# Performance work log

Hardware: AMD Instinct MI355X
Metric: run time of the kernel (lower is better)

## Reference

```python
import jax, jax.numpy as jnp
import numpy as np
from jax import lax

MARGIN_1 = 0.3
ALPHA_1 = 0.5
B, D = 256, 512
N_CLASSES = 32


def setup_inputs() -> dict:
    key = jax.random.key(0)
    k1, k2, k3 = jax.random.split(key, 3)
    feature = jax.random.normal(k1, (B, D), dtype=jnp.float32)
    sub = jax.random.randint(k2, (B,), 0, 2, dtype=jnp.int64)
    targets = jax.random.randint(k3, (B,), 0, N_CLASSES, dtype=jnp.int64)
    return {"feature": feature, "sub": sub, "targets": targets}


def _masked_softmax(logits, mask):
    # softmax over last axis restricted to `mask`; rows with empty mask -> all zeros
    # (matches torch behavior where an empty gather yields a zero transition matrix)
    neg = jnp.where(mask, logits, -jnp.inf)
    m = jnp.max(neg, axis=-1, keepdims=True)
    m = jnp.where(jnp.isfinite(m), m, 0.0)
    e = jnp.where(mask, jnp.exp(logits - m), 0.0)
    s = jnp.sum(e, axis=-1, keepdims=True)
    return e / jnp.maximum(s, 1e-30)


def _masked_mean(v, m):
    cnt = jnp.maximum(jnp.sum(m), 1).astype(v.dtype)
    return jnp.sum(jnp.where(m, v, 0.0)) / cnt


def _transition_loss(feature, sub, targets, margin_1, alpha_1):
    n = feature.shape[0]
    sim = feature @ feature.T  # [B,B], reused for every anchor

    def trans(mask_r, mask_c):
        # ab: rows -> mask_c columns; ba: rows -> mask_r columns.
        # Columns outside the mask are exactly 0, so the matmul only mixes
        # the same subset entries as torch's gathered mm, embedded in [B,B].
        ab = _masked_softmax(sim, mask_c[None, :])  # [B,B]
        ba = _masked_softmax(sim, mask_r[None, :])  # [B,B]
        tr = ab @ ba  # valid on rows/cols in mask_r
        return jnp.sqrt(jnp.clip(tr, 1e-12))

    def body(acc, i):
        is_pos = targets == targets[i]  # includes i itself
        is_neg = ~is_pos
        intra = sub == sub[i]
        cross = ~intra
        mpi = is_pos & intra
        mpc = is_pos & cross
        mni = is_neg & intra
        mnc = is_neg & cross
        trans_pos = trans(mpi, mpc)
        trans_neg = trans(mni, mnc)
        loss_ap = _masked_mean(jnp.clip(trans_neg + (margin_1 - alpha_1), 0.0),
                               mni[:, None] & mni[None, :])
        loss_an = _masked_mean(jnp.clip(alpha_1 - trans_pos, 0.0),
                               mpi[:, None] & mpi[None, :])
        return acc + loss_ap + loss_an, None

    total, _ = lax.scan(body, jnp.float32(0.0), jnp.arange(n))
    return total / n


def reference(feature, sub, targets):
    # NB: the torch module computes normalize(feature) into `x` but never uses it;
    # the loss consumes the raw `feature`, so we do the same.
    return _transition_loss(feature, sub, targets, MARGIN_1, ALPHA_1)
```

## Files before the change

### kernel.cpp

```cpp
#include <hip/hip_runtime.h>
#include <hip/hip_bf16.h>
#include <math.h>


constexpr int kB = 256;
constexpr int kD = 512;
constexpr float NEG_BIG = -3.4e38f;

typedef _Float16 f16x8 __attribute__((ext_vector_type(8)));
typedef float f32x16 __attribute__((ext_vector_type(16)));

constexpr int O_SIM = 0;
constexpr int O_M   = 262144;
constexpr int O_L   = 327680;
constexpr int O_IDX = 393216;
constexpr int O_CNT = 524288;
constexpr int O_MI  = 525312;
constexpr int O_MS  = 527360;

constexpr int XB_Q   = 43520;
constexpr int XB_E   = XB_Q + 1024;
constexpr int XB_F   = XB_E + 1024;
constexpr int XB_IK  = XB_F + 1024;
constexpr int XB_IR  = XB_IK + 512;
constexpr int XB_ROW = XB_IR + 512;
constexpr int XB_RED = XB_ROW + 8320;
constexpr int K2_LDS = XB_RED + 32;

__global__ __launch_bounds__(512)
void simStatsKernel(const float* __restrict__ f, const int* __restrict__ tgt,
                    const int* __restrict__ sub, float* __restrict__ sim,
                    float* __restrict__ Mv, float* __restrict__ Lv,
                    unsigned short* __restrict__ idxAll, int* __restrict__ cnt4,
                    int4* __restrict__ metaI, float* __restrict__ metaS,
                    float* __restrict__ out) {
  __shared__ float frow[2][512];
  __shared__ float panel[2][260];
  const int tid = threadIdx.x, lane = tid & 63, wave = tid >> 6;
  const int r0 = blockIdx.x * 2;
  if (tid < 256)
    ((float4*)frow)[tid] = ((const float4*)(f + (size_t)r0 * kD))[tid];
  __syncthreads();
  {
    const float4 a00 = *(const float4*)&frow[0][lane * 8];
    const float4 a01 = *(const float4*)&frow[0][lane * 8 + 4];
    const float4 a10 = *(const float4*)&frow[1][lane * 8];
    const float4 a11 = *(const float4*)&frow[1][lane * 8 + 4];
#pragma unroll 4
    for (int j = 0; j < 32; j++) {
      const int c = (wave << 5) | j;
      const float* fc = f + (size_t)c * kD + lane * 8;
      const float4 b0 = *(const float4*)fc;
      const float4 b1 = *(const float4*)(fc + 4);
      float d0 = 0.f, d1 = 0.f;
      d0 = fmaf(a00.x, b0.x, d0); d1 = fmaf(a10.x, b0.x, d1);
      d0 = fmaf(a00.y, b0.y, d0); d1 = fmaf(a10.y, b0.y, d1);
      d0 = fmaf(a00.z, b0.z, d0); d1 = fmaf(a10.z, b0.z, d1);
      d0 = fmaf(a00.w, b0.w, d0); d1 = fmaf(a10.w, b0.w, d1);
      d0 = fmaf(a01.x, b1.x, d0); d1 = fmaf(a11.x, b1.x, d1);
      d0 = fmaf(a01.y, b1.y, d0); d1 = fmaf(a11.y, b1.y, d1);
      d0 = fmaf(a01.z, b1.z, d0); d1 = fmaf(a11.z, b1.z, d1);
      d0 = fmaf(a01.w, b1.w, d0); d1 = fmaf(a11.w, b1.w, d1);
#pragma unroll
      for (int o = 32; o >= 1; o >>= 1) {
        d0 += __shfl_xor(d0, o, 64);
        d1 += __shfl_xor(d1, o, 64);
      }
      if (lane == 0) { panel[0][c] = d0; panel[1][c] = d1; }
    }
  }
  __syncthreads();
  if (tid < 128) {
    int rh = tid >> 6, t6 = tid & 63;
    ((float4*)(sim + (size_t)(r0 + rh) * kB))[t6] = ((const float4*)panel[rh])[t6];
  }
  {
    const int row = wave & 1, a = r0 + row;
    const float4 v4 = ((const float4*)panel[row])[lane];
    const int4 t4 = ((const int4*)tgt)[lane];
    const int4 s4 = ((const int4*)sub)[lane];
    const int ta = tgt[a], sa = sub[a];
    const int p0 = (wave >> 1) * 16;
    for (int jj = 0; jj < 16; jj++) {
      const int p = p0 + jj, t = p >> 1, s = p & 1;
      const bool pa = (ta == t), ia = (sa == s);
      const bool e0 = ((t4.x == t) == pa) && ((s4.x == s) != ia);
      const bool e1 = ((t4.y == t) == pa) && ((s4.y == s) != ia);
      const bool e2 = ((t4.z == t) == pa) && ((s4.z == s) != ia);
      const bool e3 = ((t4.w == t) == pa) && ((s4.w == s) != ia);
      float m = fmaxf(fmaxf(e0 ? v4.x : NEG_BIG, e1 ? v4.y : NEG_BIG),
                      fmaxf(e2 ? v4.z : NEG_BIG, e3 ? v4.w : NEG_BIG));
#pragma unroll
      for (int o = 32; o >= 1; o >>= 1) m = fmaxf(m, __shfl_xor(m, o, 64));
      float ss = (e0 ? __expf(v4.x - m) : 0.f) + (e1 ? __expf(v4.y - m) : 0.f)
               + (e2 ? __expf(v4.z - m) : 0.f) + (e3 ? __expf(v4.w - m) : 0.f);
#pragma unroll
      for (int o = 32; o >= 1; o >>= 1) ss += __shfl_xor(ss, o, 64);
      if (lane == 0) { Mv[p * 256 + a] = m; Lv[p * 256 + a] = __logf(ss); }
    }
  }
  if (blockIdx.x < 64 && wave == 0) {
    const int p = blockIdx.x, t = p >> 1, s = p & 1;
    int base[4] = {0, 0, 0, 0};
    for (int chunk = 0; chunk < 4; chunk++) {
      int c = chunk * 64 + lane;
      bool pos = (tgt[c] == t), intra = (sub[c] == s);
      int cat = pos ? (intra ? 0 : 1) : (intra ? 2 : 3);
#pragma unroll
      for (int l = 0; l < 4; l++) {
        bool fl = (cat == l);
        unsigned long long mm = __ballot(fl);
        if (fl) {
          int pf = __popcll(mm & ((1ull << lane) - 1ull));
          idxAll[(p * 4 + l) * 256 + base[l] + pf] = (unsigned short)c;
        }
        base[l] += __popcll(mm);
      }
    }
    if (lane == 0) {
      cnt4[p * 4 + 0] = base[0]; cnt4[p * 4 + 1] = base[1];
      cnt4[p * 4 + 2] = base[2]; cnt4[p * 4 + 3] = base[3];
      const int mult = base[0];
#pragma unroll
      for (int part = 0; part < 2; part++) {
        int nR = part ? base[0] : base[2];
        int nK = part ? base[1] : base[3];
        int KP = (nK + 15) & ~15;
        int4 mi; mi.x = nR; mi.y = nK; mi.z = KP + 8; mi.w = KP;
        metaI[p * 2 + part] = mi;
        metaS[p * 2 + part] = (mult > 0 && nR > 0 && nK > 0)
            ? (float)mult / ((float)nR * (float)nR * 256.f) : 0.f;
      }
    }
  }
  if (blockIdx.x == 64 && tid == 0) out[0] = 0.f;
}

__global__ __launch_bounds__(512)
void pairKernel(const float* __restrict__ sim, const float* __restrict__ Mv,
                const float* __restrict__ Lv, const unsigned short* __restrict__ idxAll,
                const int* __restrict__ cnt4, const int4* __restrict__ metaI,
                const float* __restrict__ metaS, float* __restrict__ out) {
  extern __shared__ char smemRaw[];
  const int pp = blockIdx.x, p = pp >> 1, part = pp & 1;
  const int tid = threadIdx.x, lane = tid & 63, wave = tid >> 6;
  const float scale = metaS[pp];
  if (scale == 0.f) {
    if (part == 1 && tid == 0) {
      int nR = cnt4[p * 4 + 0], nK = cnt4[p * 4 + 1];
      if (nR > 0 && nK == 0)
        atomicAdd(out, (float)nR * (0.5f - 1e-6f) * (1.f / 256.f));
    }
    return;
  }
  const int4 mi = metaI[pp];
  const int nR = mi.x, nK = mi.y, SKh = mi.z, KP = mi.w;
  const int nT = (nR + 31) >> 5, nRp = nT << 5;

  _Float16* Xh = (_Float16*)smemRaw;
  float* q   = (float*)(smemRaw + XB_Q);
  float* Ev  = (float*)(smemRaw + XB_E);
  float* Fv  = (float*)(smemRaw + XB_F);
  unsigned short* iKs = (unsigned short*)(smemRaw + XB_IK);
  unsigned short* iRs = (unsigned short*)(smemRaw + XB_IR);
  float* rowst = (float*)(smemRaw + XB_ROW);
  float* wred  = (float*)(smemRaw + XB_RED);

  const unsigned short* giR = idxAll + (p * 4 + (part ? 0 : 2)) * 256;
  const unsigned short* giK = idxAll + (p * 4 + (part ? 1 : 3)) * 256;
  if (tid < 256) {
    iRs[tid] = (tid < nR) ? giR[tid] : (unsigned short)0;
    int ik = (tid < nK) ? (int)giK[tid] : 0;
    iKs[tid] = (unsigned short)ik;
    q[tid] = (tid < nK) ? 0.5f * (Mv[p * 256 + ik] + Lv[p * 256 + ik]) : 0.f;
  }
  __syncthreads();

  auto loadRow = [&](int r) -> float4 {
    if (r < nR)
      return ((const float4*)(sim + (size_t)iRs[r] * kB))[lane];
    float4 z; z.x = z.y = z.z = z.w = 0.f; return z;
  };
  float4 v = loadRow(wave);
  for (int r = wave; r < nRp; r += 8) {
    float4 vn = loadRow(r + 8);
    if (r < nR) {
      *(float4*)(rowst + wave * 260 + lane * 4) = v;
      asm volatile("s_waitcnt lgkmcnt(0)" ::: "memory");
      float vals[4];
      float w = NEG_BIG;
#pragma unroll
      for (int j = 0; j < 4; j++) {
        int k = lane + 64 * j;
        float x = NEG_BIG;
        if (k < nK) x = rowst[wave * 260 + (int)iKs[k]] - q[k];
        vals[j] = x; w = fmaxf(w, x);
      }
#pragma unroll
      for (int o = 32; o >= 1; o >>= 1) w = fmaxf(w, __shfl_xor(w, o, 64));
#pragma unroll
      for (int j = 0; j < 4; j++) {
        int k = lane + 64 * j;
        if (k < KP) Xh[r * SKh + k] = (_Float16)__expf(vals[j] - w);
      }
      if (lane == 0) {
        float u = Mv[p * 256 + (int)iRs[r]] + Lv[p * 256 + (int)iRs[r]];
        Ev[r] = __expf(0.5f * (w - u));
        Fv[r] = __expf(0.5f * w);
      }
    } else {
#pragma unroll
      for (int j = 0; j < 4; j++) {
        int k = lane + 64 * j;
        if (k < KP) Xh[r * SKh + k] = (_Float16)0.f;
      }
      if (lane == 0) { Ev[r] = 0.f; Fv[r] = 0.f; }
    }
    v = vn;
  }
  __syncthreads();

  float res = 0.f;
  const int l31 = lane & 31, kg = lane >> 5;
  const int nTiles = nT * nT;
  for (int t = wave; t < nTiles; t += 8) {
    const int r0t = (t / nT) << 5, c0t = (t % nT) << 5;
    const _Float16* pa = Xh + (r0t + l31) * SKh + 8 * kg;
    const _Float16* pb = Xh + (c0t + l31) * SKh + 8 * kg;
    f32x16 acc;
#pragma unroll
    for (int g = 0; g < 16; g++) acc[g] = 0.f;
    for (int kb = 0; kb < KP; kb += 16) {
      f16x8 av = *(const f16x8*)(pa + kb);
      f16x8 bv = *(const f16x8*)(pb + kb);
      acc = __builtin_amdgcn_mfma_f32_32x32x16_f16(av, bv, acc, 0, 0, 0);
    }
    const int c = c0t + l31;
    if (c < nR) {
      const float Fc = Fv[c];
      const int rb = r0t + 4 * kg;
#pragma unroll
      for (int g = 0; g < 16; g++) {
        const int r = rb + (g & 3) + ((g >> 2) << 3);
        if (r < nR) {
          float x = Ev[r] * Fc * sqrtf(acc[g]);
          x = fmaxf(x, 1e-6f);
          res += part ? fmaxf(0.5f - x, 0.f) : fmaxf(x - 0.2f, 0.f);
        }
      }
    }
  }
#pragma unroll
  for (int o = 32; o >= 1; o >>= 1) res += __shfl_xor(res, o, 64);
  if (lane == 0) wred[wave] = res;
  __syncthreads();
  if (tid == 0) {
    float tot = 0.f;
#pragma unroll
    for (int w2 = 0; w2 < 8; w2++) tot += wred[w2];
    atomicAdd(out, tot * scale);
  }
}

extern "C" void kernel_launch(void* const* d_in, const int* in_sizes, int n_in,
                              void* d_out, int out_size, void* d_ws, size_t ws_size,
                              hipStream_t stream) {
  (void)in_sizes; (void)n_in; (void)out_size; (void)ws_size;
  const float* feature = (const float*)d_in[0];
  const int* subv = (const int*)d_in[1];
  const int* tgtv = (const int*)d_in[2];
  float* out = (float*)d_out;
  char* ws = (char*)d_ws;

  float* sim = (float*)(ws + O_SIM);
  float* Mv = (float*)(ws + O_M);
  float* Lv = (float*)(ws + O_L);
  unsigned short* idxAll = (unsigned short*)(ws + O_IDX);
  int* cnt4 = (int*)(ws + O_CNT);
  int4* metaI = (int4*)(ws + O_MI);
  float* metaS = (float*)(ws + O_MS);

  simStatsKernel<<<128, 512, 0, stream>>>(feature, tgtv, subv, sim, Mv, Lv,
                                          idxAll, cnt4, metaI, metaS, out);
  pairKernel<<<128, 512, K2_LDS, stream>>>(sim, Mv, Lv, idxAll, cnt4,
                                           metaI, metaS, out);
}
```

Measured before the change: 107.2 us.

## Fuse sim/stats and pair kernels into one cooperative kernel with grid sync

Merges the two kernel launches into a single cooperative kernel: each block computes its sim rows, softmax stats and index lists, then a grid-wide barrier separates this from the pair/transition phase, which now uses static shared memory. The goal is to remove the second launch and the inter-kernel gap. In exchange it relies on all 128 blocks being co-resident and pays for a grid sync, and the phase-2 LDS footprint is now reserved statically for the whole kernel.

```diff
diff --git a/kernel.cpp b/kernel.cpp
--- a/kernel.cpp
+++ b/kernel.cpp
@@ -1,7 +1,10 @@
 #include <hip/hip_runtime.h>
 #include <hip/hip_bf16.h>
+#include <hip/hip_cooperative_groups.h>
 #include <math.h>
 
+
+namespace cg = cooperative_groups;
 
 constexpr int kB = 256;
 constexpr int kD = 512;
@@ -10,13 +13,13 @@
 typedef _Float16 f16x8 __attribute__((ext_vector_type(8)));
 typedef float f32x16 __attribute__((ext_vector_type(16)));
 
-constexpr int O_SIM = 0;
-constexpr int O_M   = 262144;
-constexpr int O_L   = 327680;
-constexpr int O_IDX = 393216;
-constexpr int O_CNT = 524288;
-constexpr int O_MI  = 525312;
-constexpr int O_MS  = 527360;
+constexpr int O_SIM   = 0;
+constexpr int O_M     = 262144;
+constexpr int O_L     = 327680;
+constexpr int O_IDX   = 393216;
+constexpr int O_CNT   = 524288;
+constexpr int O_MI    = 525312;
+constexpr int O_MS    = 527360;
 
 constexpr int XB_Q   = 43520;
 constexpr int XB_E   = XB_Q + 1024;
@@ -25,125 +28,124 @@
 constexpr int XB_IR  = XB_IK + 512;
 constexpr int XB_ROW = XB_IR + 512;
 constexpr int XB_RED = XB_ROW + 8320;
-constexpr int K2_LDS = XB_RED + 32;
+constexpr int SMEM_SZ = XB_RED + 32;
 
 __global__ __launch_bounds__(512)
-void simStatsKernel(const float* __restrict__ f, const int* __restrict__ tgt,
-                    const int* __restrict__ sub, float* __restrict__ sim,
-                    float* __restrict__ Mv, float* __restrict__ Lv,
-                    unsigned short* __restrict__ idxAll, int* __restrict__ cnt4,
-                    int4* __restrict__ metaI, float* __restrict__ metaS,
-                    float* __restrict__ out) {
-  __shared__ float frow[2][512];
-  __shared__ float panel[2][260];
+void fusedKernel(const float* __restrict__ f, const int* __restrict__ tgt,
+                 const int* __restrict__ sub, float* __restrict__ sim,
+                 float* __restrict__ Mv, float* __restrict__ Lv,
+                 unsigned short* __restrict__ idxAll, int* __restrict__ cnt4,
+                 int4* __restrict__ metaI, float* __restrict__ metaS,
+                 float* __restrict__ out) {
+  __shared__ __align__(16) char smem[SMEM_SZ];
   const int tid = threadIdx.x, lane = tid & 63, wave = tid >> 6;
-  const int r0 = blockIdx.x * 2;
-  if (tid < 256)
-    ((float4*)frow)[tid] = ((const float4*)(f + (size_t)r0 * kD))[tid];
-  __syncthreads();
+  const int b = blockIdx.x;
+
   {
-    const float4 a00 = *(const float4*)&frow[0][lane * 8];
-    const float4 a01 = *(const float4*)&frow[0][lane * 8 + 4];
-    const float4 a10 = *(const float4*)&frow[1][lane * 8];
-    const float4 a11 = *(const float4*)&frow[1][lane * 8 + 4];
+    float (*frow)[512] = (float (*)[512])smem;
+    float (*panel)[260] = (float (*)[260])(smem + 4096);
+    const int r0 = b * 2;
+    if (tid < 256)
+      ((float4*)frow)[tid] = ((const float4*)(f + (size_t)r0 * kD))[tid];
+    __syncthreads();
+    {
+      const float4 a00 = *(const float4*)&frow[0][lane * 8];
+      const float4 a01 = *(const float4*)&frow[0][lane * 8 + 4];
+      const float4 a10 = *(const float4*)&frow[1][lane * 8];
+      const float4 a11 = *(const float4*)&frow[1][lane * 8 + 4];
 #pragma unroll 4
-    for (int j = 0; j < 32; j++) {
-      const int c = (wave << 5) | j;
-      const float* fc = f + (size_t)c * kD + lane * 8;
-      const float4 b0 = *(const float4*)fc;
-      const float4 b1 = *(const float4*)(fc + 4);
-      float d0 = 0.f, d1 = 0.f;
-      d0 = fmaf(a00.x, b0.x, d0); d1 = fmaf(a10.x, b0.x, d1);
-      d0 = fmaf(a00.y, b0.y, d0); d1 = fmaf(a10.y, b0.y, d1);
-      d0 = fmaf(a00.z, b0.z, d0); d1 = fmaf(a10.z, b0.z, d1);
-      d0 = fmaf(a00.w, b0.w, d0); d1 = fmaf(a10.w, b0.w, d1);
-      d0 = fmaf(a01.x, b1.x, d0); d1 = fmaf(a11.x, b1.x, d1);
-      d0 = fmaf(a01.y, b1.y, d0); d1 = fmaf(a11.y, b1.y, d1);
-      d0 = fmaf(a01.z, b1.z, d0); d1 = fmaf(a11.z, b1.z, d1);
-      d0 = fmaf(a01.w, b1.w, d0); d1 = fmaf(a11.w, b1.w, d1);
-#pragma unroll
-      for (int o = 32; o >= 1; o >>= 1) {
-        d0 += __shfl_xor(d0, o, 64);
-        d1 += __shfl_xor(d1, o, 64);
-      }
-      if (lane == 0) { panel[0][c] = d0; panel[1][c] = d1; }
-    }
-  }
-  __syncthreads();
-  if (tid < 128) {
-    int rh = tid >> 6, t6 = tid & 63;
-    ((float4*)(sim + (size_t)(r0 + rh) * kB))[t6] = ((const float4*)panel[rh])[t6];
-  }
-  {
-    const int row = wave & 1, a = r0 + row;
-    const float4 v4 = ((const float4*)panel[row])[lane];
-    const int4 t4 = ((const int4*)tgt)[lane];
-    const int4 s4 = ((const int4*)sub)[lane];
-    const int ta = tgt[a], sa = sub[a];
-    const int p0 = (wave >> 1) * 16;
-    for (int jj = 0; jj < 16; jj++) {
-      const int p = p0 + jj, t = p >> 1, s = p & 1;
-      const bool pa = (ta == t), ia = (sa == s);
-      const bool e0 = ((t4.x == t) == pa) && ((s4.x == s) != ia);
-      const bool e1 = ((t4.y == t) == pa) && ((s4.y == s) != ia);
-      const bool e2 = ((t4.z == t) == pa) && ((s4.z == s) != ia);
-      const bool e3 = ((t4.w == t) == pa) && ((s4.w == s) != ia);
-      float m = fmaxf(fmaxf(e0 ? v4.x : NEG_BIG, e1 ? v4.y : NEG_BIG),
-                      fmaxf(e2 ? v4.z : NEG_BIG, e3 ? v4.w : NEG_BIG));
-#pragma unroll
-      for (int o = 32; o >= 1; o >>= 1) m = fmaxf(m, __shfl_xor(m, o, 64));
-      float ss = (e0 ? __expf(v4.x - m) : 0.f) + (e1 ? __expf(v4.y - m) : 0.f)
-               + (e2 ? __expf(v4.z - m) : 0.f) + (e3 ? __expf(v4.w - m) : 0.f);
-#pragma unroll
-      for (int o = 32; o >= 1; o >>= 1) ss += __shfl_xor(ss, o, 64);
-      if (lane == 0) { Mv[p * 256 + a] = m; Lv[p * 256 + a] = __logf(ss); }
-    }
-  }
-  if (blockIdx.x < 64 && wave == 0) {
-    const int p = blockIdx.x, t = p >> 1, s = p & 1;
-    int base[4] = {0, 0, 0, 0};
-    for (int chunk = 0; chunk < 4; chunk++) {
-      int c = chunk * 64 + lane;
-      bool pos = (tgt[c] == t), intra = (sub[c] == s);
-      int cat = pos ? (intra ? 0 : 1) : (intra ? 2 : 3);
-#pragma unroll
-      for (int l = 0; l < 4; l++) {
-        bool fl = (cat == l);
-        unsigned long long mm = __ballot(fl);
-        if (fl) {
-          int pf = __popcll(mm & ((1ull << lane) - 1ull));
-          idxAll[(p * 4 + l) * 256 + base[l] + pf] = (unsigned short)c;
-        }
-        base[l] += __popcll(mm);
-      }
-    }
-    if (lane == 0) {
-      cnt4[p * 4 + 0] = base[0]; cnt4[p * 4 + 1] = base[1];
-      cnt4[p * 4 + 2] = base[2]; cnt4[p * 4 + 3] = base[3];
-      const int mult = base[0];
-#pragma unroll
-      for (int part = 0; part < 2; part++) {
-        int nR = part ? base[0] : base[2];
-        int nK = part ? base[1] : base[3];
-        int KP = (nK + 15) & ~15;
-        int4 mi; mi.x = nR; mi.y = nK; mi.z = KP + 8; mi.w = KP;
-        metaI[p * 2 + part] = mi;
-        metaS[p * 2 + part] = (mult > 0 && nR > 0 && nK > 0)
-            ? (float)mult / ((float)nR * (float)nR * 256.f) : 0.f;
-      }
-    }
-  }
-  if (blockIdx.x == 64 && tid == 0) out[0] = 0.f;
-}
-
-__global__ __launch_bounds__(512)
-void pairKernel(const float* __restrict__ sim, const float* __restrict__ Mv,
-                const float* __restrict__ Lv, const unsigned short* __restrict__ idxAll,
-                const int* __restrict__ cnt4, const int4* __restrict__ metaI,
-                const float* __restrict__ metaS, float* __restrict__ out) {
-  extern __shared__ char smemRaw[];
-  const int pp = blockIdx.x, p = pp >> 1, part = pp & 1;
-  const int tid = threadIdx.x, lane = tid & 63, wave = tid >> 6;
+      for (int j = 0; j < 32; j++) {
+        const int c = (wave << 5) | j;
+        const float* fc = f + (size_t)c * kD + lane * 8;
+        const float4 b0 = *(const float4*)fc;
+        const float4 b1 = *(const float4*)(fc + 4);
+        float d0 = 0.f, d1 = 0.f;
+        d0 = fmaf(a00.x, b0.x, d0); d1 = fmaf(a10.x, b0.x, d1);
+        d0 = fmaf(a00.y, b0.y, d0); d1 = fmaf(a10.y, b0.y, d1);
+        d0 = fmaf(a00.z, b0.z, d0); d1 = fmaf(a10.z, b0.z, d1);
+        d0 = fmaf(a00.w, b0.w, d0); d1 = fmaf(a10.w, b0.w, d1);
+        d0 = fmaf(a01.x, b1.x, d0); d1 = fmaf(a11.x, b1.x, d1);
+        d0 = fmaf(a01.y, b1.y, d0); d1 = fmaf(a11.y, b1.y, d1);
+        d0 = fmaf(a01.z, b1.z, d0); d1 = fmaf(a11.z, b1.z, d1);
+        d0 = fmaf(a01.w, b1.w, d0); d1 = fmaf(a11.w, b1.w, d1);
+#pragma unroll
+        for (int o = 32; o >= 1; o >>= 1) {
+          d0 += __shfl_xor(d0, o, 64);
+          d1 += __shfl_xor(d1, o, 64);
+        }
+        if (lane == 0) { panel[0][c] = d0; panel[1][c] = d1; }
+      }
+    }
+    __syncthreads();
+    if (tid < 128) {
+      int rh = tid >> 6, t6 = tid & 63;
+      ((float4*)(sim + (size_t)(r0 + rh) * kB))[t6] = ((const float4*)panel[rh])[t6];
+    }
+    {
+      const int row = wave & 1, a = r0 + row;
+      const float4 v4 = ((const float4*)panel[row])[lane];
+      const int4 t4 = ((const int4*)tgt)[lane];
+      const int4 s4 = ((const int4*)sub)[lane];
+      const int ta = tgt[a], sa = sub[a];
+      const int p0 = (wave >> 1) * 16;
+      for (int jj = 0; jj < 16; jj++) {
+        const int p = p0 + jj, t = p >> 1, s = p & 1;
+        const bool pa = (ta == t), ia = (sa == s);
+        const bool e0 = ((t4.x == t) == pa) && ((s4.x == s) != ia);
+        const bool e1 = ((t4.y == t) == pa) && ((s4.y == s) != ia);
+        const bool e2 = ((t4.z == t) == pa) && ((s4.z == s) != ia);
+        const bool e3 = ((t4.w == t) == pa) && ((s4.w == s) != ia);
+        float m = fmaxf(fmaxf(e0 ? v4.x : NEG_BIG, e1 ? v4.y : NEG_BIG),
+                        fmaxf(e2 ? v4.z : NEG_BIG, e3 ? v4.w : NEG_BIG));
+#pragma unroll
+        for (int o = 32; o >= 1; o >>= 1) m = fmaxf(m, __shfl_xor(m, o, 64));
+        float ss = (e0 ? __expf(v4.x - m) : 0.f) + (e1 ? __expf(v4.y - m) : 0.f)
+                 + (e2 ? __expf(v4.z - m) : 0.f) + (e3 ? __expf(v4.w - m) : 0.f);
+#pragma unroll
+        for (int o = 32; o >= 1; o >>= 1) ss += __shfl_xor(ss, o, 64);
+        if (lane == 0) { Mv[p * 256 + a] = m; Lv[p * 256 + a] = __logf(ss); }
+      }
+    }
+    if (b < 64 && wave == 0) {
+      const int p = b, t = p >> 1, s = p & 1;
+      int base[4] = {0, 0, 0, 0};
+      for (int chunk = 0; chunk < 4; chunk++) {
+        int c = chunk * 64 + lane;
+        bool pos = (tgt[c] == t), intra = (sub[c] == s);
+        int cat = pos ? (intra ? 0 : 1) : (intra ? 2 : 3);
+#pragma unroll
+        for (int l = 0; l < 4; l++) {
+          bool fl = (cat == l);
+          unsigned long long mm = __ballot(fl);
+          if (fl) {
+            int pf = __popcll(mm & ((1ull << lane) - 1ull));
+            idxAll[(p * 4 + l) * 256 + base[l] + pf] = (unsigned short)c;
+          }
+          base[l] += __popcll(mm);
+        }
+      }
+      if (lane == 0) {
+        cnt4[p * 4 + 0] = base[0]; cnt4[p * 4 + 1] = base[1];
+        cnt4[p * 4 + 2] = base[2]; cnt4[p * 4 + 3] = base[3];
+        const int mult = base[0];
+#pragma unroll
+        for (int part = 0; part < 2; part++) {
+          int nR = part ? base[0] : base[2];
+          int nK = part ? base[1] : base[3];
+          int KP = (nK + 15) & ~15;
+          int4 mi; mi.x = nR; mi.y = nK; mi.z = KP + 8; mi.w = KP;
+          metaI[p * 2 + part] = mi;
+          metaS[p * 2 + part] = (mult > 0 && nR > 0 && nK > 0)
+              ? (float)mult / ((float)nR * (float)nR * 256.f) : 0.f;
+        }
+      }
+    }
+    if (b == 64 && tid == 0) out[0] = 0.f;
+  }
+
+  cg::this_grid().sync();
+
+  const int pp = b, p = pp >> 1, part = pp & 1;
   const float scale = metaS[pp];
   if (scale == 0.f) {
     if (part == 1 && tid == 0) {
@@ -157,14 +159,14 @@
   const int nR = mi.x, nK = mi.y, SKh = mi.z, KP = mi.w;
   const int nT = (nR + 31) >> 5, nRp = nT << 5;
 
-  _Float16* Xh = (_Float16*)smemRaw;
-  float* q   = (float*)(smemRaw + XB_Q);
-  float* Ev  = (float*)(smemRaw + XB_E);
-  float* Fv  = (float*)(smemRaw + XB_F);
-  unsigned short* iKs = (unsigned short*)(smemRaw + XB_IK);
-  unsigned short* iRs = (unsigned short*)(smemRaw + XB_IR);
-  float* rowst = (float*)(smemRaw + XB_ROW);
-  float* wred  = (float*)(smemRaw + XB_RED);
+  _Float16* Xh = (_Float16*)smem;
+  float* q   = (float*)(smem + XB_Q);
+  float* Ev  = (float*)(smem + XB_E);
+  float* Fv  = (float*)(smem + XB_F);
+  unsigned short* iKs = (unsigned short*)(smem + XB_IK);
+  unsigned short* iRs = (unsigned short*)(smem + XB_IR);
+  float* rowst = (float*)(smem + XB_ROW);
+  float* wred  = (float*)(smem + XB_RED);
 
   const unsigned short* giR = idxAll + (p * 4 + (part ? 0 : 2)) * 256;
   const unsigned short* giK = idxAll + (p * 4 + (part ? 1 : 3)) * 256;
@@ -280,8 +282,9 @@
   int4* metaI = (int4*)(ws + O_MI);
   float* metaS = (float*)(ws + O_MS);
 
-  simStatsKernel<<<128, 512, 0, stream>>>(feature, tgtv, subv, sim, Mv, Lv,
-                                          idxAll, cnt4, metaI, metaS, out);
-  pairKernel<<<128, 512, K2_LDS, stream>>>(sim, Mv, Lv, idxAll, cnt4,
-                                           metaI, metaS, out);
+  void* args[] = { (void*)&feature, (void*)&tgtv, (void*)&subv, (void*)&sim,
+                   (void*)&Mv, (void*)&Lv, (void*)&idxAll, (void*)&cnt4,
+                   (void*)&metaI, (void*)&metaS, (void*)&out };
+  (void)hipLaunchCooperativeKernel((const void*)fusedKernel, dim3(128),
+                                   dim3(512), args, 0, stream);
 }
```

New measurement: 135.2 us. 26.1% more time.
